# Performance work log

Measured on AMD Instinct MI355X. Metric: run time of the kernel, lower is better.

Reference implementation:

```python
import jax, jax.numpy as jnp
import numpy as np

ROPE_THETA = 10000.0
NUM_HEADS = 16


def apply_rope(x, pos, theta=ROPE_THETA):
    # x: [b, h, s, d_h]; pos: [s] int positions
    d = x.shape[-1]
    inv_freq = 1.0 / (theta ** (jnp.arange(0, d, 2, dtype=jnp.float32) / d))  # [d/2]
    ang = pos.astype(jnp.float32)[:, None] * inv_freq[None, :]  # [s, d/2]
    cos, sin = jnp.cos(ang), jnp.sin(ang)
    x1, x2 = x[..., 0::2], x[..., 1::2]  # interleaved pairs
    r1 = x1 * cos - x2 * sin
    r2 = x1 * sin + x2 * cos
    return jnp.stack([r1, r2], axis=-1).reshape(x.shape)


def setup_inputs() -> dict:
    key = jax.random.key(0)
    k1, k2, k3 = jax.random.split(key, 3)
    B, S, D = 4, 2048, 1024
    x = jax.random.normal(k1, (B, S, D), dtype=jnp.float32)
    W_qkv = jax.random.normal(k2, (3, D, D), dtype=jnp.float32) * 0.02
    W_o = jax.random.normal(k3, (D, D), dtype=jnp.float32) * 0.02
    token_positions = jnp.arange(S, dtype=jnp.int32)
    return {"x": x, "W_qkv": W_qkv, "W_o": W_o, "token_positions": token_positions}


def reference(x, W_qkv, W_o, token_positions):
    B, S, D = x.shape
    H = NUM_HEADS
    dh = D // H
    # fused QKV projection: [3, b, s, d]
    qkv = jnp.einsum('bsd,kod->kbso', x, W_qkv)
    # split heads: [3, b, h, s, d_h]
    qkv = qkv.reshape(3, B, S, H, dh).transpose(0, 1, 3, 2, 4)
    q, k, v = qkv[0], qkv[1], qkv[2]
    q = apply_rope(q, token_positions)
    k = apply_rope(k, token_positions)
    scores = jnp.einsum('bhqd,bhkd->bhqk', q, k) / jnp.sqrt(jnp.float32(dh))
    causal = jnp.tril(jnp.ones((S, S), dtype=bool))
    scores = jnp.where(causal, scores, jnp.finfo(scores.dtype).min)
    probs = jax.nn.softmax(scores, axis=-1)
    out = jnp.einsum('bhqk,bhkd->bhqd', probs, v)
    out = out.transpose(0, 2, 1, 3).reshape(B, S, D)  # merge heads
    return out @ W_o.T
```

## Files before the change

kernel.cpp:

```cpp
#include <hip/hip_runtime.h>

typedef unsigned short ushort_t;
typedef unsigned int uint_t;
typedef __bf16 bf16_t;
typedef bf16_t bf16x8 __attribute__((ext_vector_type(8)));
typedef float floatx4 __attribute__((ext_vector_type(4)));

typedef const __attribute__((address_space(1))) uint_t* gptr_t;
typedef __attribute__((address_space(3))) uint_t* lptr_t;

#define BATCH 4
#define SEQ   2048
#define DMODEL 1024
#define NHEAD 16
#define DH    64
#define BHSD  (BATCH*NHEAD*SEQ*DH)
#define QSCALE 0.18033688f
#define MFIX2  11.5415603f

__device__ __forceinline__ float b2f(ushort_t u) {
    uint_t x = ((uint_t)u) << 16;
    return __uint_as_float(x);
}
__device__ __forceinline__ ushort_t f2b(float f) {
    uint_t u = __float_as_uint(f);
    u = (u + 0x7fffu + ((u >> 16) & 1u)) >> 16;
    return (ushort_t)u;
}

__global__ __launch_bounds__(256) void cast_kernel(
    const float* __restrict__ in, ushort_t* __restrict__ out, int n)
{
    int i = (blockIdx.x * 256 + threadIdx.x) * 4;
    if (i >= n) return;
    float4 v = *(const float4*)&in[i];
    ushort4 o;
    o.x = f2b(v.x); o.y = f2b(v.y); o.z = f2b(v.z); o.w = f2b(v.w);
    *(ushort4*)&out[i] = o;
}

__global__ void rope_table_kernel(const int* __restrict__ tp,
                                  float* __restrict__ ct,
                                  float* __restrict__ st) {
    int idx = blockIdx.x * 256 + threadIdx.x;
    int s = idx >> 5;
    int i = idx & 31;
    float pos = (float)tp[s];
    float invf = expf(-(float)i * 0.28782313662425572f);
    float ang = pos * invf;
    float sv, cv;
    sincosf(ang, &sv, &cv);
    ct[idx] = cv;
    st[idx] = sv;
}

__device__ __forceinline__ void gemm_bt_tile(
    const ushort_t* __restrict__ A, const ushort_t* __restrict__ B, int K,
    int mbase, int nbase, floatx4 acc[4][4],
    ushort_t* __restrict__ As, ushort_t* __restrict__ Bs)
{
    const int tid  = threadIdx.x;
    const int lane = tid & 63;
    const int wave = tid >> 6;
    const int wm   = (wave >> 1) << 6;
    const int wn   = (wave & 1) << 6;
    const int quad = lane >> 4;
    const int l16  = lane & 15;
    const int lrow = lane >> 3;
    const int lcol = (((lane & 7) ^ lrow) << 3);
    const int rsw  = l16 & 7;

#pragma unroll
    for (int mi = 0; mi < 4; mi++)
#pragma unroll
        for (int ni = 0; ni < 4; ni++)
            acc[mi][ni] = (floatx4){0.f, 0.f, 0.f, 0.f};

    for (int k0 = 0; k0 < K; k0 += 64) {
        __syncthreads();
#pragma unroll
        for (int c = 0; c < 4; ++c) {
            int chunk = wave * 4 + c;
            int row = chunk * 8 + lrow;
            __builtin_amdgcn_global_load_lds(
                (gptr_t)&A[(size_t)(mbase + row) * K + k0 + lcol],
                (lptr_t)&As[chunk * 512], 16, 0, 0);
            __builtin_amdgcn_global_load_lds(
                (gptr_t)&B[(size_t)(nbase + row) * K + k0 + lcol],
                (lptr_t)&Bs[chunk * 512], 16, 0, 0);
        }
        __syncthreads();

#pragma unroll
        for (int kq = 0; kq < 2; ++kq) {
            const int cg = ((kq * 4 + quad) ^ rsw) * 8;
            bf16x8 af[4], bfr[4];
#pragma unroll
            for (int i = 0; i < 4; i++)
                af[i]  = *(const bf16x8*)&As[(wm + i * 16 + l16) * 64 + cg];
#pragma unroll
            for (int i = 0; i < 4; i++)
                bfr[i] = *(const bf16x8*)&Bs[(wn + i * 16 + l16) * 64 + cg];

#pragma unroll
            for (int mi = 0; mi < 4; mi++)
#pragma unroll
                for (int ni = 0; ni < 4; ni++)
                    acc[mi][ni] = __builtin_amdgcn_mfma_f32_16x16x32_bf16(
                        af[mi], bfr[ni], acc[mi][ni], 0, 0, 0);
        }
    }
}

__global__ __launch_bounds__(256) void qkv_rope_kernel(
    const ushort_t* __restrict__ x, const ushort_t* __restrict__ Wqkv,
    const float* __restrict__ ctab, const float* __restrict__ stab,
    ushort_t* __restrict__ qkv)
{
    __shared__ __align__(16) ushort_t As[128 * 64];
    __shared__ __align__(16) ushort_t Bs[128 * 64];
    __shared__ __align__(16) ushort_t T[32 * 136];
    floatx4 acc[4][4];

    const int which = blockIdx.z;
    const int mbase = blockIdx.x * 128;
    const int nbase = blockIdx.y * 128;

    gemm_bt_tile(x, Wqkv + (size_t)which * DMODEL * DMODEL, DMODEL,
                 mbase, nbase, acc, As, Bs);

    const int tid  = threadIdx.x;
    const int lane = tid & 63;
    const int wave = tid >> 6;
    const int wm = (wave >> 1) << 6, wn = (wave & 1) << 6;
    const int quad = lane >> 4, l16 = lane & 15;
    const int wrow0 = (wm ? 16 : 0) + quad * 4;

    for (int mi = 0; mi < 4; mi++) {
#pragma unroll
        for (int ni = 0; ni < 4; ni++) {
#pragma unroll
            for (int r = 0; r < 4; r++) {
                int grow = mbase + wm + mi * 16 + quad * 4 + r;
                int gcol = nbase + wn + ni * 16 + l16;
                float val = acc[mi][ni][r];
                float partner = __shfl_xor(val, 1);
                int s  = grow & (SEQ - 1);
                int dd = gcol & (DH - 1);
                float res = val;
                if (which < 2) {
                    int fi = dd >> 1;
                    float cs = ctab[s * 32 + fi];
                    float sn = stab[s * 32 + fi];
                    res = (gcol & 1) ? fmaf(partner, sn, val * cs)
                                     : fmaf(val, cs, -partner * sn);
                }
                if (which == 0) res *= QSCALE;
                T[(wrow0 + r) * 136 + wn + ni * 16 + l16] = f2b(res);
            }
        }
        __syncthreads();

#pragma unroll
        for (int cc = 0; cc < 2; ++cc) {
            int c = cc * 256 + tid;
            int q2 = c >> 7, ci = c & 127;
            int rgrp = q2 >> 1, hh = q2 & 1;
            int growb = mbase + rgrp * 64;
            int bb = growb >> 11;
            int hidx = (nbase >> 6) + hh;
            size_t bufb = ((size_t)bb * NHEAD + hidx) * ((size_t)SEQ * DH);
            if (which == 0) {
                int row16 = ci >> 3, dd8 = (ci & 7) << 3;
                int s = (growb & (SEQ - 1)) + mi * 16 + row16;
                uint4 d = *(const uint4*)&T[(rgrp * 16 + row16) * 136 + hh * 64 + dd8];
                *(uint4*)&qkv[bufb + (size_t)s * DH + dd8] = d;
            } else {
                int kt = (growb & (SEQ - 1)) >> 6;
                if (which == 1) {
                    int kc = ci >> 6, rem = ci & 63;
                    int qd = rem >> 4, lk = rem & 15;
                    int cflat = (kc * 4 + mi) * 64 + qd * 16 + lk;
                    uint4 d = *(const uint4*)&T[(rgrp * 16 + lk) * 136 + hh * 64 + kc * 32 + qd * 8];
                    *(uint4*)&qkv[(size_t)BHSD + bufb + (size_t)kt * 4096 + cflat * 8] = d;
                } else {
                    int tt = ci >> 6, rem = ci & 63;
                    int nd = rem >> 4, lv = rem & 15;
                    int cflat = ((mi >> 1) * 4 + nd) * 64 + ((mi * 2 + tt) & 3) * 16 + lv;
                    ushort_t tmp[8];
#pragma unroll
                    for (int j = 0; j < 8; ++j)
                        tmp[j] = T[(rgrp * 16 + tt * 8 + j) * 136 + hh * 64 + nd * 16 + lv];
                    *(uint4*)&qkv[2 * (size_t)BHSD + bufb + (size_t)kt * 4096 + cflat * 8]
                        = *(uint4*)tmp;
                }
            }
        }
        __syncthreads();
    }
}

__global__ __launch_bounds__(64) void attn_mfma_kernel(
    const ushort_t* __restrict__ q, const ushort_t* __restrict__ kf,
    const ushort_t* __restrict__ vf, ushort_t* __restrict__ attnout)
{
    __shared__ __align__(16) ushort_t Pw[32 * 72];

    const int lane = threadIdx.x;
    const int quad = lane >> 4;
    const int l16  = lane & 15;
    const int bid = blockIdx.x;
    const int bh = (bid & 7) * 8 + ((bid >> 3) & 7);
    const int chunk = 63 - (bid >> 6);
    const int b = bh >> 4, h = bh & 15;
    const size_t base = (size_t)bh * SEQ * DH;
    const int q0w = chunk * 32;

    bf16x8 qf[2][2];
#pragma unroll
    for (int mi = 0; mi < 2; mi++)
#pragma unroll
        for (int kc = 0; kc < 2; kc++)
            qf[mi][kc] = *(const bf16x8*)&q[base
                + (size_t)(q0w + mi * 16 + l16) * DH + kc * 32 + quad * 8];

    floatx4 o[2][4];
    float lp[2][4];
#pragma unroll
    for (int mi = 0; mi < 2; mi++)
#pragma unroll
        for (int nd = 0; nd < 4; nd++)
            o[mi][nd] = (floatx4){0.f, 0.f, 0.f, 0.f};
#pragma unroll
    for (int mi = 0; mi < 2; mi++)
#pragma unroll
        for (int r = 0; r < 4; r++)
            lp[mi][r] = 0.f;

    const int ktmax = (q0w + 31) >> 6;

    bf16x8 kfr[2][4];
#pragma unroll
    for (int kc = 0; kc < 2; kc++)
#pragma unroll
        for (int ni = 0; ni < 4; ni++)
            kfr[kc][ni] = *(const bf16x8*)&kf[base + (kc * 4 + ni) * 512 + lane * 8];

    for (int kt = 0; kt <= ktmax; ++kt) {
        const ushort_t* vtb = &vf[base + (size_t)kt * 4096];
        const int ktn = (kt < ktmax) ? kt + 1 : ktmax;
        const ushort_t* knb = &kf[base + (size_t)ktn * 4096];

        floatx4 s[2][4];
#pragma unroll
        for (int mi = 0; mi < 2; mi++)
#pragma unroll
            for (int ni = 0; ni < 4; ni++)
                s[mi][ni] = (floatx4){0.f, 0.f, 0.f, 0.f};
#pragma unroll
        for (int kc = 0; kc < 2; kc++)
#pragma unroll
            for (int mi = 0; mi < 2; mi++)
#pragma unroll
                for (int ni = 0; ni < 4; ni++)
                    s[mi][ni] = __builtin_amdgcn_mfma_f32_16x16x32_bf16(
                        qf[mi][kc], kfr[kc][ni], s[mi][ni], 0, 0, 0);

        bf16x8 vfr[2][4];
#pragma unroll
        for (int kc = 0; kc < 2; kc++)
#pragma unroll
            for (int nd = 0; nd < 4; nd++)
                vfr[kc][nd] = *(const bf16x8*)&vtb[(kc * 4 + nd) * 512 + lane * 8];

#pragma unroll
        for (int kc = 0; kc < 2; kc++)
#pragma unroll
            for (int ni = 0; ni < 4; ni++)
                kfr[kc][ni] = *(const bf16x8*)&knb[(kc * 4 + ni) * 512 + lane * 8];

        const bool needs_mask = (kt == ktmax);

#pragma unroll
        for (int mi = 0; mi < 2; mi++) {
#pragma unroll
            for (int r = 0; r < 4; r++) {
                if (needs_mask) {
                    int row_g = q0w + mi * 16 + quad * 4 + r;
#pragma unroll
                    for (int ni = 0; ni < 4; ni++) {
                        int col_g = kt * 64 + ni * 16 + l16;
                        s[mi][ni][r] = (col_g <= row_g) ? s[mi][ni][r]
                                                        : -INFINITY;
                    }
                }
                float accv = 0.f;
#pragma unroll
                for (int ni = 0; ni < 4; ni++) {
                    float p = exp2f(s[mi][ni][r] - MFIX2);
                    s[mi][ni][r] = p;
                    accv += p;
                }
                lp[mi][r] += accv;
            }
        }

#pragma unroll
        for (int mi = 0; mi < 2; mi++)
#pragma unroll
            for (int ni = 0; ni < 4; ni++)
#pragma unroll
                for (int r = 0; r < 4; r++)
                    Pw[(mi * 16 + quad * 4 + r) * 72 + ni * 16 + l16]
                        = f2b(s[mi][ni][r]);

#pragma unroll
        for (int kc = 0; kc < 2; kc++) {
            bf16x8 pf[2];
#pragma unroll
            for (int mi = 0; mi < 2; mi++)
                pf[mi] = *(const bf16x8*)&Pw[(mi * 16 + l16) * 72 + kc * 32 + quad * 8];
#pragma unroll
            for (int mi = 0; mi < 2; mi++)
#pragma unroll
                for (int nd = 0; nd < 4; nd++)
                    o[mi][nd] = __builtin_amdgcn_mfma_f32_16x16x32_bf16(
                        pf[mi], vfr[kc][nd], o[mi][nd], 0, 0, 0);
        }
    }

#pragma unroll
    for (int mi = 0; mi < 2; mi++)
#pragma unroll
        for (int r = 0; r < 4; r++) {
            float lf = lp[mi][r];
            lf += __shfl_xor(lf, 1);
            lf += __shfl_xor(lf, 2);
            lf += __shfl_xor(lf, 4);
            lf += __shfl_xor(lf, 8);
            lp[mi][r] = 1.0f / lf;
        }
#pragma unroll
    for (int mi = 0; mi < 2; mi++)
#pragma unroll
        for (int nd = 0; nd < 4; nd++)
#pragma unroll
            for (int r = 0; r < 4; r++) {
                int s_idx = q0w + mi * 16 + quad * 4 + r;
                float val = o[mi][nd][r] * lp[mi][r];
                attnout[((size_t)(b * SEQ + s_idx)) * DMODEL + h * DH + nd * 16 + l16]
                    = f2b(val);
            }
}

#define ASL(pa,h) (((pa)*2+(h))*8192)
#define BSL(pa,h) (32768 + ((pa)*2+(h))*8192)

#define RD_A(pa, mh)                                                        \
    {                                                                       \
        const int ab_ = ASL(pa, wr);                                        \
        _Pragma("unroll")                                                   \
        for (int mm = 0; mm < 4; ++mm) {                                    \
            afr[mm][0] = *(const bf16x8*)&lds[ab_ + (((mh)*4+mm)*16 + l16)*64 + cg0]; \
            afr[mm][1] = *(const bf16x8*)&lds[ab_ + (((mh)*4+mm)*16 + l16)*64 + cg1]; \
        }                                                                   \
    }

#define RD_B(pa, nh, BS_)                                                   \
    {                                                                       \
        const int bb_ = BSL(pa, (wc >> 1));                                 \
        _Pragma("unroll")                                                   \
        for (int nn = 0; nn < 2; ++nn) {                                    \
            const int rowl_ = (wc & 1) * 64 + ((nh)*2+nn)*16 + l16;         \
            BS_[nn][0] = *(const bf16x8*)&lds[bb_ + rowl_*64 + cg0];        \
            BS_[nn][1] = *(const bf16x8*)&lds[bb_ + rowl_*64 + cg1];        \
        }                                                                   \
    }

#define MM(mh, nh, BS_)                                                     \
    {                                                                       \
        _Pragma("unroll")                                                   \
        for (int mm = 0; mm < 4; ++mm)                                      \
        _Pragma("unroll")                                                   \
        for (int nn = 0; nn < 2; ++nn) {                                    \
            acc[(mh)*4+mm][(nh)*2+nn] = __builtin_amdgcn_mfma_f32_16x16x32_bf16( \
                afr[mm][0], BS_[nn][0], acc[(mh)*4+mm][(nh)*2+nn], 0, 0, 0);     \
            acc[(mh)*4+mm][(nh)*2+nn] = __builtin_amdgcn_mfma_f32_16x16x32_bf16( \
                afr[mm][1], BS_[nn][1], acc[(mh)*4+mm][(nh)*2+nn], 0, 0, 0);     \
        }                                                                   \
    }

#define PH_ENTER() do {                                                     \
        asm volatile("s_barrier" ::: "memory");                             \
        asm volatile("s_waitcnt lgkmcnt(0)" ::: "memory");                  \
        __builtin_amdgcn_sched_barrier(0);                                  \
        __builtin_amdgcn_s_setprio(1); } while (0)

#define PH_EXIT() do {                                                      \
        __builtin_amdgcn_s_setprio(0);                                      \
        __builtin_amdgcn_sched_barrier(0);                                  \
        asm volatile("s_barrier" ::: "memory"); } while (0)

__device__ __forceinline__ void gemm256_core(
    const ushort_t* __restrict__ Ag, const ushort_t* __restrict__ Bg, int K,
    int mbase, int nbase, floatx4 acc[8][4], ushort_t* lds)
{
    const int tid  = threadIdx.x;
    const int lane = tid & 63;
    const int wave = tid >> 6;
    const int wr   = wave >> 2;
    const int wc   = wave & 3;
    const int quad = lane >> 4;
    const int l16  = lane & 15;
    const int cg0  = ((quad)     ^ (l16 & 7)) * 8;
    const int cg1  = ((4 + quad) ^ (l16 & 7)) * 8;
    const int rl0  = tid >> 3;
    const int scol = ((tid & 7) ^ (rl0 & 7)) << 3;

#pragma unroll
    for (int m = 0; m < 8; ++m)
#pragma unroll
        for (int n = 0; n < 4; ++n)
            acc[m][n] = (floatx4){0.f, 0.f, 0.f, 0.f};

    bf16x8 afr[4][2], bs0[2][2], bs1[2][2];

#define STAGE(srcp, slotb, growb, kk)                                       \
    {                                                                       \
        _Pragma("unroll")                                                   \
        for (int v = 0; v < 2; ++v)                                         \
            __builtin_amdgcn_global_load_lds(                               \
                (gptr_t)&(srcp)[(size_t)((growb) + v*64 + rl0) * K + (kk) + scol], \
                (lptr_t)&lds[(slotb) + v*4096 + wave*512 + lane*8], 16, 0, 0);     \
    }

    STAGE(Bg, BSL(0,0), nbase,       0);
    STAGE(Bg, BSL(0,1), nbase + 128, 0);
    STAGE(Ag, ASL(0,0), mbase,       0);
    STAGE(Ag, ASL(0,1), mbase + 128, 0);
    STAGE(Bg, BSL(1,0), nbase,       64);
    STAGE(Bg, BSL(1,1), nbase + 128, 64);
    asm volatile("s_waitcnt vmcnt(4)" ::: "memory");
    asm volatile("s_barrier" ::: "memory");

    const int NIT = K >> 7;
    for (int it = 0; it < NIT; ++it) {
        const int t0k = it << 7;
        const int t1k = t0k + 64;
        const bool last = (it == NIT - 1);

        RD_A(0, 0); RD_B(0, 0, bs0);
        STAGE(Ag, ASL(1,0), mbase, t1k);
        PH_ENTER(); MM(0, 0, bs0); PH_EXIT();
        RD_B(0, 1, bs1);
        STAGE(Ag, ASL(1,1), mbase + 128, t1k);
        PH_ENTER(); MM(0, 1, bs1); PH_EXIT();
        RD_A(0, 1);
        if (!last) STAGE(Bg, BSL(0,0), nbase, t0k + 128);
        PH_ENTER(); MM(1, 0, bs0); PH_EXIT();
        if (!last) {
            STAGE(Bg, BSL(0,1), nbase + 128, t0k + 128);
            asm volatile("s_waitcnt vmcnt(4)" ::: "memory");
        } else {
            asm volatile("s_waitcnt vmcnt(0)" ::: "memory");
        }
        PH_ENTER(); MM(1, 1, bs1); PH_EXIT();
        RD_A(1, 0); RD_B(1, 0, bs0);
        if (!last) STAGE(Ag, ASL(0,0), mbase, t0k + 128);
        PH_ENTER(); MM(0, 0, bs0); PH_EXIT();
        RD_B(1, 1, bs1);
        if (!last) STAGE(Ag, ASL(0,1), mbase + 128, t0k + 128);
        PH_ENTER(); MM(0, 1, bs1); PH_EXIT();
        RD_A(1, 1);
        if (!last) STAGE(Bg, BSL(1,0), nbase, t1k + 128);
        PH_ENTER(); MM(1, 0, bs0); PH_EXIT();
        if (!last) {
            STAGE(Bg, BSL(1,1), nbase + 128, t1k + 128);
            asm volatile("s_waitcnt vmcnt(4)" ::: "memory");
        }
        PH_ENTER(); MM(1, 1, bs1); PH_EXIT();
    }
#undef STAGE
}

__global__ __launch_bounds__(512, 2) void outproj_kernel(
    const ushort_t* __restrict__ Ain, const ushort_t* __restrict__ Wo,
    float* __restrict__ out)
{
    __shared__ __align__(16) ushort_t lds[65536];
    floatx4 acc[8][4];

    const int mbase = blockIdx.x * 256;
    const int nbase = blockIdx.y * 256;
    gemm256_core(Ain, Wo, DMODEL, mbase, nbase, acc, lds);

    const int lane = threadIdx.x & 63;
    const int wave = threadIdx.x >> 6;
    const int wr = wave >> 2, wc = wave & 3;
    const int quad = lane >> 4, l16 = lane & 15;

#pragma unroll
    for (int m = 0; m < 8; ++m)
#pragma unroll
        for (int n = 0; n < 4; ++n)
#pragma unroll
            for (int r = 0; r < 4; ++r) {
                int grow = mbase + wr * 128 + m * 16 + quad * 4 + r;
                int gcol = nbase + wc * 64 + n * 16 + l16;
                out[(size_t)grow * DMODEL + gcol] = acc[m][n][r];
            }
}

extern "C" void kernel_launch(void* const* d_in, const int* in_sizes, int n_in,
                              void* d_out, int out_size, void* d_ws, size_t ws_size,
                              hipStream_t stream) {
    const float* x_f    = (const float*)d_in[0];
    const float* Wqkv_f = (const float*)d_in[1];
    const float* Wo_f   = (const float*)d_in[2];
    const int* tp       = (const int*)d_in[3];
    float* out          = (float*)d_out;

    char* ws = (char*)d_ws;
    ushort_t* qkv     = (ushort_t*)(ws);
    ushort_t* attnout = (ushort_t*)(ws + 50331648);
    float* ctab       = (float*)(ws + 67108864);
    float* stab       = (float*)(ws + 67371008);
    ushort_t* xb      = (ushort_t*)(ws + 67633152);
    ushort_t* Wqkvb   = (ushort_t*)(ws + 84410368);
    ushort_t* Wob     = (ushort_t*)(ws + 90701824);

    const int n_x  = BATCH * SEQ * DMODEL;
    const int n_wq = 3 * DMODEL * DMODEL;
    const int n_wo = DMODEL * DMODEL;

    cast_kernel<<<dim3(n_x  / 1024), dim3(256), 0, stream>>>(x_f,    xb,    n_x);
    cast_kernel<<<dim3(n_wq / 1024), dim3(256), 0, stream>>>(Wqkv_f, Wqkvb, n_wq);
    cast_kernel<<<dim3(n_wo / 1024), dim3(256), 0, stream>>>(Wo_f,   Wob,   n_wo);

    rope_table_kernel<<<dim3(SEQ * 32 / 256), dim3(256), 0, stream>>>(tp, ctab, stab);

    qkv_rope_kernel<<<dim3(BATCH * SEQ / 128, DMODEL / 128, 3), dim3(256), 0, stream>>>(
        xb, Wqkvb, ctab, stab, qkv);

    attn_mfma_kernel<<<dim3(4096), dim3(64), 0, stream>>>(
        qkv, qkv + (size_t)BHSD, qkv + 2 * (size_t)BHSD, attnout);

    outproj_kernel<<<dim3(BATCH * SEQ / 256, DMODEL / 256), dim3(512), 0, stream>>>(
        attnout, Wob, out);
}
```

Measured before the change: 284.7 us.

## Share K/V tiles across four waves via double-buffered LDS in attention

The attention kernel now runs 4 waves per block, each handling a 32-row query chunk of the same head. K and V tiles are staged once per block into double-buffered shared memory with global_load_lds and read by all four waves, instead of each single-wave block loading K/V straight from global into registers. This cuts redundant global and L2 traffic by sharing each tile, and overlaps the next tile's load with compute. The cost is block-wide barriers every tile and idle waves on the causal tail, since waves with earlier queries finish their key range sooner but still wait at the barriers.

```diff
diff --git a/kernel.cpp b/kernel.cpp
--- a/kernel.cpp
+++ b/kernel.cpp
@@ -200,21 +200,29 @@
     }
 }
 
-__global__ __launch_bounds__(64) void attn_mfma_kernel(
+__global__ __launch_bounds__(256, 2) void attn_mfma_kernel(
     const ushort_t* __restrict__ q, const ushort_t* __restrict__ kf,
     const ushort_t* __restrict__ vf, ushort_t* __restrict__ attnout)
 {
-    __shared__ __align__(16) ushort_t Pw[32 * 72];
-
-    const int lane = threadIdx.x;
+    __shared__ __align__(16) ushort_t Kb[2][4096];
+    __shared__ __align__(16) ushort_t Vb[2][4096];
+    __shared__ __align__(16) ushort_t Pw[4][32 * 72];
+
+    const int tid  = threadIdx.x;
+    const int lane = tid & 63;
+    const int wave = tid >> 6;
     const int quad = lane >> 4;
     const int l16  = lane & 15;
-    const int bid = blockIdx.x;
-    const int bh = (bid & 7) * 8 + ((bid >> 3) & 7);
-    const int chunk = 63 - (bid >> 6);
+    const int bid  = blockIdx.x;
+    const int bh   = (bid & 7) * 8 + ((bid >> 3) & 7);
+    const int cg   = 15 - (bid >> 6);
     const int b = bh >> 4, h = bh & 15;
     const size_t base = (size_t)bh * SEQ * DH;
+    const int chunk = cg * 4 + wave;
     const int q0w = chunk * 32;
+    const int ktmax_w = (q0w + 31) >> 6;
+    const int ktmax_b = 2 * cg + 1;
+    ushort_t* Pme = Pw[wave];
 
     bf16x8 qf[2][2];
 #pragma unroll
@@ -237,97 +245,106 @@
         for (int r = 0; r < 4; r++)
             lp[mi][r] = 0.f;
 
-    const int ktmax = (q0w + 31) >> 6;
-
-    bf16x8 kfr[2][4];
-#pragma unroll
-    for (int kc = 0; kc < 2; kc++)
-#pragma unroll
-        for (int ni = 0; ni < 4; ni++)
-            kfr[kc][ni] = *(const bf16x8*)&kf[base + (kc * 4 + ni) * 512 + lane * 8];
-
-    for (int kt = 0; kt <= ktmax; ++kt) {
-        const ushort_t* vtb = &vf[base + (size_t)kt * 4096];
-        const int ktn = (kt < ktmax) ? kt + 1 : ktmax;
-        const ushort_t* knb = &kf[base + (size_t)ktn * 4096];
-
-        floatx4 s[2][4];
-#pragma unroll
-        for (int mi = 0; mi < 2; mi++)
-#pragma unroll
-            for (int ni = 0; ni < 4; ni++)
-                s[mi][ni] = (floatx4){0.f, 0.f, 0.f, 0.f};
-#pragma unroll
-        for (int kc = 0; kc < 2; kc++)
+#define ATTN_STAGE(p, t)                                                    \
+    {                                                                       \
+        const ushort_t* kt_ = &kf[base + (size_t)(t) * 4096];               \
+        const ushort_t* vt_ = &vf[base + (size_t)(t) * 4096];               \
+        __builtin_amdgcn_global_load_lds((gptr_t)&kt_[tid * 8],             \
+            (lptr_t)&Kb[p][wave * 512], 16, 0, 0);                          \
+        __builtin_amdgcn_global_load_lds((gptr_t)&kt_[2048 + tid * 8],      \
+            (lptr_t)&Kb[p][2048 + wave * 512], 16, 0, 0);                   \
+        __builtin_amdgcn_global_load_lds((gptr_t)&vt_[tid * 8],             \
+            (lptr_t)&Vb[p][wave * 512], 16, 0, 0);                          \
+        __builtin_amdgcn_global_load_lds((gptr_t)&vt_[2048 + tid * 8],      \
+            (lptr_t)&Vb[p][2048 + wave * 512], 16, 0, 0);                   \
+    }
+
+    ATTN_STAGE(0, 0);
+
+    for (int kt = 0; kt <= ktmax_b; ++kt) {
+        const int p = kt & 1;
+        ATTN_STAGE(p ^ 1, (kt < ktmax_b) ? kt + 1 : ktmax_b);
+        asm volatile("s_waitcnt vmcnt(4)" ::: "memory");
+        __builtin_amdgcn_s_barrier();
+
+        if (kt <= ktmax_w) {
+            floatx4 s[2][4];
 #pragma unroll
             for (int mi = 0; mi < 2; mi++)
 #pragma unroll
                 for (int ni = 0; ni < 4; ni++)
-                    s[mi][ni] = __builtin_amdgcn_mfma_f32_16x16x32_bf16(
-                        qf[mi][kc], kfr[kc][ni], s[mi][ni], 0, 0, 0);
-
-        bf16x8 vfr[2][4];
-#pragma unroll
-        for (int kc = 0; kc < 2; kc++)
-#pragma unroll
-            for (int nd = 0; nd < 4; nd++)
-                vfr[kc][nd] = *(const bf16x8*)&vtb[(kc * 4 + nd) * 512 + lane * 8];
-
-#pragma unroll
-        for (int kc = 0; kc < 2; kc++)
-#pragma unroll
-            for (int ni = 0; ni < 4; ni++)
-                kfr[kc][ni] = *(const bf16x8*)&knb[(kc * 4 + ni) * 512 + lane * 8];
-
-        const bool needs_mask = (kt == ktmax);
-
-#pragma unroll
-        for (int mi = 0; mi < 2; mi++) {
-#pragma unroll
-            for (int r = 0; r < 4; r++) {
-                if (needs_mask) {
-                    int row_g = q0w + mi * 16 + quad * 4 + r;
+                    s[mi][ni] = (floatx4){0.f, 0.f, 0.f, 0.f};
+#pragma unroll
+            for (int kc = 0; kc < 2; kc++) {
+                bf16x8 kfr[4];
+#pragma unroll
+                for (int ni = 0; ni < 4; ni++)
+                    kfr[ni] = *(const bf16x8*)&Kb[p][(kc * 4 + ni) * 512 + lane * 8];
+#pragma unroll
+                for (int mi = 0; mi < 2; mi++)
+#pragma unroll
+                    for (int ni = 0; ni < 4; ni++)
+                        s[mi][ni] = __builtin_amdgcn_mfma_f32_16x16x32_bf16(
+                            qf[mi][kc], kfr[ni], s[mi][ni], 0, 0, 0);
+            }
+
+            const bool needs_mask = (kt == ktmax_w);
+
+#pragma unroll
+            for (int mi = 0; mi < 2; mi++) {
+#pragma unroll
+                for (int r = 0; r < 4; r++) {
+                    if (needs_mask) {
+                        int row_g = q0w + mi * 16 + quad * 4 + r;
+#pragma unroll
+                        for (int ni = 0; ni < 4; ni++) {
+                            int col_g = kt * 64 + ni * 16 + l16;
+                            s[mi][ni][r] = (col_g <= row_g) ? s[mi][ni][r]
+                                                            : -INFINITY;
+                        }
+                    }
+                    float accv = 0.f;
 #pragma unroll
                     for (int ni = 0; ni < 4; ni++) {
-                        int col_g = kt * 64 + ni * 16 + l16;
-                        s[mi][ni][r] = (col_g <= row_g) ? s[mi][ni][r]
-                                                        : -INFINITY;
+                        float pv = exp2f(s[mi][ni][r] - MFIX2);
+                        s[mi][ni][r] = pv;
+                        accv += pv;
                     }
+                    lp[mi][r] += accv;
                 }
-                float accv = 0.f;
-#pragma unroll
-                for (int ni = 0; ni < 4; ni++) {
-                    float p = exp2f(s[mi][ni][r] - MFIX2);
-                    s[mi][ni][r] = p;
-                    accv += p;
-                }
-                lp[mi][r] += accv;
-            }
-        }
-
-#pragma unroll
-        for (int mi = 0; mi < 2; mi++)
-#pragma unroll
-            for (int ni = 0; ni < 4; ni++)
-#pragma unroll
-                for (int r = 0; r < 4; r++)
-                    Pw[(mi * 16 + quad * 4 + r) * 72 + ni * 16 + l16]
-                        = f2b(s[mi][ni][r]);
-
-#pragma unroll
-        for (int kc = 0; kc < 2; kc++) {
-            bf16x8 pf[2];
+            }
+
 #pragma unroll
             for (int mi = 0; mi < 2; mi++)
-                pf[mi] = *(const bf16x8*)&Pw[(mi * 16 + l16) * 72 + kc * 32 + quad * 8];
-#pragma unroll
-            for (int mi = 0; mi < 2; mi++)
+#pragma unroll
+                for (int ni = 0; ni < 4; ni++)
+#pragma unroll
+                    for (int r = 0; r < 4; r++)
+                        Pme[(mi * 16 + quad * 4 + r) * 72 + ni * 16 + l16]
+                            = f2b(s[mi][ni][r]);
+
+#pragma unroll
+            for (int kc = 0; kc < 2; kc++) {
+                bf16x8 pf[2];
+#pragma unroll
+                for (int mi = 0; mi < 2; mi++)
+                    pf[mi] = *(const bf16x8*)&Pme[(mi * 16 + l16) * 72 + kc * 32 + quad * 8];
+                bf16x8 vfr[4];
 #pragma unroll
                 for (int nd = 0; nd < 4; nd++)
-                    o[mi][nd] = __builtin_amdgcn_mfma_f32_16x16x32_bf16(
-                        pf[mi], vfr[kc][nd], o[mi][nd], 0, 0, 0);
-        }
-    }
+                    vfr[nd] = *(const bf16x8*)&Vb[p][(kc * 4 + nd) * 512 + lane * 8];
+#pragma unroll
+                for (int mi = 0; mi < 2; mi++)
+#pragma unroll
+                    for (int nd = 0; nd < 4; nd++)
+                        o[mi][nd] = __builtin_amdgcn_mfma_f32_16x16x32_bf16(
+                            pf[mi], vfr[nd], o[mi][nd], 0, 0, 0);
+            }
+        }
+        __builtin_amdgcn_s_barrier();
+    }
+#undef ATTN_STAGE
+    asm volatile("s_waitcnt vmcnt(0)" ::: "memory");
 
 #pragma unroll
     for (int mi = 0; mi < 2; mi++)
@@ -542,7 +559,7 @@
     qkv_rope_kernel<<<dim3(BATCH * SEQ / 128, DMODEL / 128, 3), dim3(256), 0, stream>>>(
         xb, Wqkvb, ctab, stab, qkv);
 
-    attn_mfma_kernel<<<dim3(4096), dim3(64), 0, stream>>>(
+    attn_mfma_kernel<<<dim3(1024), dim3(256), 0, stream>>>(
         qkv, qkv + (size_t)BHSD, qkv + 2 * (size_t)BHSD, attnout);
 
     outproj_kernel<<<dim3(BATCH * SEQ / 256, DMODEL / 256), dim3(512), 0, stream>>>(
```

After: 288.3 us. About the same (+1.3%).
